# Kernel tuning notes

Hardware: AMD Instinct MI355X
Metric: run time of the kernel (lower is better)

Reference implementation:

```python
import jax, jax.numpy as jnp
import numpy as np

BN_EPS = 1e-5


def setup_inputs() -> dict:
    key = jax.random.key(0)
    ks = jax.random.split(key, 10)
    B, L, V, D = 4096, 200, 100000, 256
    tokens = jax.random.randint(ks[0], (B, L), 0, V, dtype=jnp.int32)
    lengths = jnp.maximum(jax.random.randint(ks[1], (B,), 0, L + 1, dtype=jnp.int32), 1)
    t = (jax.random.uniform(ks[2], (B,)) > 0.5).astype(jnp.float32)
    emb_table = jax.random.normal(ks[3], (V, D), dtype=jnp.float32)
    W1 = jax.random.normal(ks[4], (D, D), dtype=jnp.float32) * (1.0 / np.sqrt(D))
    b1 = jnp.zeros((D,), dtype=jnp.float32)
    gamma = jnp.ones((D,), dtype=jnp.float32)
    beta = jnp.zeros((D,), dtype=jnp.float32)
    w2 = jax.random.normal(ks[5], (D,), dtype=jnp.float32) * (1.0 / np.sqrt(D))
    b2 = jnp.zeros((), dtype=jnp.float32)
    return {"tokens": tokens, "lengths": lengths, "t": t, "emb_table": emb_table,
            "W1": W1, "b1": b1, "gamma": gamma, "beta": beta, "w2": w2, "b2": b2}


def reference(tokens, lengths, t, emb_table, W1, b1, gamma, beta, w2, b2):
    B, L = tokens.shape
    # ragged gather + mean pool (EmbeddingBag-mean equivalent)
    emb = emb_table[tokens]                                   # [B, L, D]
    mask = (jnp.arange(L)[None, :] < lengths[:, None]).astype(emb.dtype)  # [B, L]
    pooled = jnp.einsum('bld,bl->bd', emb, mask) / lengths[:, None].astype(emb.dtype)
    # fc_hidden -> BatchNorm1d (training-mode batch stats) -> ReLU (dropout = eval identity)
    z = pooled @ W1.T + b1                                    # [B, D]
    mu = jnp.mean(z, axis=0)
    var = jnp.var(z, axis=0)
    zn = (z - mu) / jnp.sqrt(var + BN_EPS)
    h = jax.nn.relu(gamma * zn + beta)
    # fc_output -> logits
    logits = h @ w2 + b2                                      # [B]
    # BCEWithLogitsLoss (mean, numerically stable)
    loss = jnp.mean(jnp.maximum(logits, 0.0) - logits * t + jnp.log1p(jnp.exp(-jnp.abs(logits))))
    return (loss, logits)
```

## Files before the change

### kernel.cpp

```cpp
#include <hip/hip_runtime.h>
#include <math.h>

#define L_ 200

__global__ __launch_bounds__(256) void pool_pack_kernel(
    const int* __restrict__ tokens, const int* __restrict__ lengths,
    const float* __restrict__ emb, float* __restrict__ pooled,
    const float* __restrict__ W1, float* __restrict__ W1p) {
  const int tid = threadIdx.x;
  if (blockIdx.x < 64) {
    float4 v = ((const float4*)W1)[tid * 64 + blockIdx.x];
    ((float4*)W1p)[blockIdx.x * 256 + tid] = v;
  }
  const int wv = tid >> 6, lane = tid & 63;
  const int row = blockIdx.x * 2 + (wv >> 1);
  const int half = wv & 1;
  const int len = lengths[row];
  const int* trow = tokens + row * L_;
  const float4* embv = (const float4*)emb;
  float4 a0 = make_float4(0.f, 0.f, 0.f, 0.f);
  float4 a1 = a0, a2 = a0, a3 = a0;
  for (int l0 = half * 64; l0 < len; l0 += 128) {
    int nt = len - l0; nt = nt > 64 ? 64 : nt;
    int tk = (lane < nt) ? trow[l0 + lane] : 0;
    int j = 0;
    for (; j + 4 <= nt; j += 4) {
      int t0 = __shfl(tk, j);
      int t1 = __shfl(tk, j + 1);
      int t2 = __shfl(tk, j + 2);
      int t3 = __shfl(tk, j + 3);
      float4 v0 = embv[(size_t)t0 * 64 + lane];
      float4 v1 = embv[(size_t)t1 * 64 + lane];
      float4 v2 = embv[(size_t)t2 * 64 + lane];
      float4 v3 = embv[(size_t)t3 * 64 + lane];
      a0.x += v0.x; a0.y += v0.y; a0.z += v0.z; a0.w += v0.w;
      a1.x += v1.x; a1.y += v1.y; a1.z += v1.z; a1.w += v1.w;
      a2.x += v2.x; a2.y += v2.y; a2.z += v2.z; a2.w += v2.w;
      a3.x += v3.x; a3.y += v3.y; a3.z += v3.z; a3.w += v3.w;
    }
    for (; j < nt; j++) {
      int t0 = __shfl(tk, j);
      float4 v0 = embv[(size_t)t0 * 64 + lane];
      a0.x += v0.x; a0.y += v0.y; a0.z += v0.z; a0.w += v0.w;
    }
  }
  float4 r;
  r.x = a0.x + a1.x + a2.x + a3.x;
  r.y = a0.y + a1.y + a2.y + a3.y;
  r.z = a0.z + a1.z + a2.z + a3.z;
  r.w = a0.w + a1.w + a2.w + a3.w;
  __shared__ float4 part[2][64];
  if (half) part[wv >> 1][lane] = r;
  __syncthreads();
  if (!half) {
    float4 o = part[wv >> 1][lane];
    const float inv = 1.0f / (float)len;
    r.x = (r.x + o.x) * inv;
    r.y = (r.y + o.y) * inv;
    r.z = (r.z + o.z) * inv;
    r.w = (r.w + o.w) * inv;
    ((float4*)pooled)[(size_t)row * 64 + lane] = r;
  }
}

__global__ __launch_bounds__(256) void gemm_stats_kernel(
    const float* __restrict__ pooled, const float* __restrict__ W1p,
    const float* __restrict__ b1, float* __restrict__ z,
    float* __restrict__ psum, float* __restrict__ psq) {
  __shared__ float4 SH[1024];
  const int tid = threadIdx.x;
  const int b0 = blockIdx.x * 16;
  const float4* pooled4 = (const float4*)pooled;
#pragma unroll
  for (int i = 0; i < 4; i++)
    SH[tid + i * 256] = pooled4[(size_t)b0 * 64 + tid + i * 256];
  __syncthreads();
  const int wv = tid >> 6, lane = tid & 63;
  const int r0 = wv * 4;
  float4 bb = ((const float4*)b1)[lane];
  float acc[4][4];
#pragma unroll
  for (int r = 0; r < 4; r++) {
    acc[r][0] = bb.x; acc[r][1] = bb.y; acc[r][2] = bb.z; acc[r][3] = bb.w;
  }
  const float4* w4 = (const float4*)W1p;
  for (int kb = 0; kb < 64; kb++) {
    float4 wk0 = w4[kb * 256 + lane * 4 + 0];
    float4 wk1 = w4[kb * 256 + lane * 4 + 1];
    float4 wk2 = w4[kb * 256 + lane * 4 + 2];
    float4 wk3 = w4[kb * 256 + lane * 4 + 3];
#pragma unroll
    for (int r = 0; r < 4; r++) {
      float4 p = SH[(r0 + r) * 64 + kb];
      acc[r][0] += p.x * wk0.x + p.y * wk0.y + p.z * wk0.z + p.w * wk0.w;
      acc[r][1] += p.x * wk1.x + p.y * wk1.y + p.z * wk1.z + p.w * wk1.w;
      acc[r][2] += p.x * wk2.x + p.y * wk2.y + p.z * wk2.z + p.w * wk2.w;
      acc[r][3] += p.x * wk3.x + p.y * wk3.y + p.z * wk3.z + p.w * wk3.w;
    }
  }
  float4* z4 = (float4*)z;
  float4 s = make_float4(0.f, 0.f, 0.f, 0.f), q = s;
#pragma unroll
  for (int r = 0; r < 4; r++) {
    float4 o = make_float4(acc[r][0], acc[r][1], acc[r][2], acc[r][3]);
    z4[(size_t)(b0 + r0 + r) * 64 + lane] = o;
    s.x += o.x; s.y += o.y; s.z += o.z; s.w += o.w;
    q.x += o.x * o.x; q.y += o.y * o.y; q.z += o.z * o.z; q.w += o.w * o.w;
  }
  __syncthreads();
  SH[wv * 64 + lane] = s;
  SH[256 + wv * 64 + lane] = q;
  __syncthreads();
  if (tid < 64) {
    float4 S = make_float4(0.f, 0.f, 0.f, 0.f), Q = S;
#pragma unroll
    for (int w = 0; w < 4; w++) {
      float4 a = SH[w * 64 + tid];
      float4 b = SH[256 + w * 64 + tid];
      S.x += a.x; S.y += a.y; S.z += a.z; S.w += a.w;
      Q.x += b.x; Q.y += b.y; Q.z += b.z; Q.w += b.w;
    }
    ((float4*)psum)[blockIdx.x * 64 + tid] = S;
    ((float4*)psq)[blockIdx.x * 64 + tid] = Q;
  }
}

__global__ __launch_bounds__(256) void bn_reduce_kernel(
    const float* __restrict__ psum, const float* __restrict__ psq,
    const float* __restrict__ gamma, const float* __restrict__ beta,
    float* __restrict__ A, float* __restrict__ C) {
  const int t = threadIdx.x;
  const int dd = t & 15, c = t >> 4;
  const int d = blockIdx.x * 16 + dd;
  float s = 0.f, q = 0.f;
#pragma unroll
  for (int i = 0; i < 16; i++) {
    int p = c * 16 + i;
    s += psum[p * 256 + d];
    q += psq[p * 256 + d];
  }
  __shared__ float sl[16][17], ql[16][17];
  sl[c][dd] = s; ql[c][dd] = q;
  __syncthreads();
  if (t < 16) {
    float S = 0.f, Q = 0.f;
#pragma unroll
    for (int c2 = 0; c2 < 16; c2++) { S += sl[c2][t]; Q += ql[c2][t]; }
    int dg = blockIdx.x * 16 + t;
    float m = S * (1.0f / 4096.0f);
    float v = Q * (1.0f / 4096.0f) - m * m;
    float a = gamma[dg] * rsqrtf(v + 1e-5f);
    A[dg] = a;
    C[dg] = beta[dg] - m * a;
  }
}

__global__ __launch_bounds__(256) void head_kernel(
    const float* __restrict__ z, const float* __restrict__ A,
    const float* __restrict__ C, const float* __restrict__ w2,
    const float* __restrict__ b2, const float* __restrict__ t,
    float* __restrict__ out, float* __restrict__ bce) {
  const int tid = threadIdx.x;
  const int wv = tid >> 6, lane = tid & 63;
  const int b = blockIdx.x * 4 + wv;
  float4 A4 = ((const float4*)A)[lane];
  float4 C4 = ((const float4*)C)[lane];
  float4 w24 = ((const float4*)w2)[lane];
  float4 zv = ((const float4*)z)[(size_t)b * 64 + lane];
  float h0 = fmaxf(A4.x * zv.x + C4.x, 0.f);
  float h1 = fmaxf(A4.y * zv.y + C4.y, 0.f);
  float h2 = fmaxf(A4.z * zv.z + C4.z, 0.f);
  float h3 = fmaxf(A4.w * zv.w + C4.w, 0.f);
  float part = h0 * w24.x + h1 * w24.y + h2 * w24.z + h3 * w24.w;
#pragma unroll
  for (int off = 32; off > 0; off >>= 1) part += __shfl_down(part, off);
  if (lane == 0) {
    float logit = part + b2[0];
    out[1 + b] = logit;
    float tb = t[b];
    bce[b] = fmaxf(logit, 0.f) - logit * tb + log1pf(expf(-fabsf(logit)));
  }
}

__global__ __launch_bounds__(256) void loss_kernel(const float* __restrict__ bce,
                                                   float* __restrict__ out) {
  __shared__ float red[4];
  const int tid = threadIdx.x;
  float s = 0.f;
  for (int i = 0; i < 16; i++) s += bce[tid + i * 256];
#pragma unroll
  for (int off = 32; off > 0; off >>= 1) s += __shfl_down(s, off);
  if ((tid & 63) == 0) red[tid >> 6] = s;
  __syncthreads();
  if (tid == 0) out[0] = (red[0] + red[1] + red[2] + red[3]) * (1.0f / 4096.0f);
}

extern "C" void kernel_launch(void* const* d_in, const int* in_sizes, int n_in,
                              void* d_out, int out_size, void* d_ws, size_t ws_size,
                              hipStream_t stream) {
  const int* tokens = (const int*)d_in[0];
  const int* lengths = (const int*)d_in[1];
  const float* t = (const float*)d_in[2];
  const float* emb = (const float*)d_in[3];
  const float* W1 = (const float*)d_in[4];
  const float* b1 = (const float*)d_in[5];
  const float* gamma = (const float*)d_in[6];
  const float* beta = (const float*)d_in[7];
  const float* w2 = (const float*)d_in[8];
  const float* b2 = (const float*)d_in[9];
  float* out = (float*)d_out;

  float* wsf = (float*)d_ws;
  float* pooled = wsf;
  float* z = wsf + 1048576;
  float* W1p = wsf + 2097152;
  float* psum = wsf + 2162688;
  float* psq = wsf + 2228224;
  float* A = wsf + 2293760;
  float* C = wsf + 2294016;
  float* bce = wsf + 2294272;

  pool_pack_kernel<<<2048, 256, 0, stream>>>(tokens, lengths, emb, pooled, W1, W1p);
  gemm_stats_kernel<<<256, 256, 0, stream>>>(pooled, W1p, b1, z, psum, psq);
  bn_reduce_kernel<<<16, 256, 0, stream>>>(psum, psq, gamma, beta, A, C);
  head_kernel<<<1024, 256, 0, stream>>>(z, A, C, w2, b2, t, out, bce);
  loss_kernel<<<1, 256, 0, stream>>>(bce, out);
}
```

Before: 240.8 us.

## Convert embedding table to bf16 each call and fuse BN reduce and loss via atomics

Adds a pass that converts the full fp32 embedding table to bf16 in workspace on every call, then gathers bf16 rows during pooling to halve the gather bytes. The BN statistics reduction and the loss reduction move to atomicAdd, which removes the separate bn_reduce and loss kernels. The conversion reads 102MB and writes 51MB per call, which likely costs more than the roughly 205MB of fp32 gathers it saves. It also lowers embedding precision and makes the float atomic sums order-dependent.

```diff
diff --git a/kernel.cpp b/kernel.cpp
--- a/kernel.cpp
+++ b/kernel.cpp
@@ -3,21 +3,54 @@
 
 #define L_ 200
 
-__global__ __launch_bounds__(256) void pool_pack_kernel(
-    const int* __restrict__ tokens, const int* __restrict__ lengths,
-    const float* __restrict__ emb, float* __restrict__ pooled,
-    const float* __restrict__ W1, float* __restrict__ W1p) {
+__device__ __forceinline__ unsigned f2bf_pair(float a, float b) {
+  union { float f; unsigned u; } ca, cb;
+  ca.f = a; cb.f = b;
+  unsigned ra = (ca.u + 0x7FFFu + ((ca.u >> 16) & 1u)) >> 16;
+  unsigned rb = (cb.u + 0x7FFFu + ((cb.u >> 16) & 1u)) >> 16;
+  return (ra & 0xFFFFu) | ((rb & 0xFFFFu) << 16);
+}
+
+__device__ __forceinline__ float bf_lo(unsigned u) {
+  union { unsigned u; float f; } c; c.u = u << 16; return c.f;
+}
+__device__ __forceinline__ float bf_hi(unsigned u) {
+  union { unsigned u; float f; } c; c.u = u & 0xFFFF0000u; return c.f;
+}
+
+__global__ __launch_bounds__(256) void convert_pack_kernel(
+    const float* __restrict__ emb, uint2* __restrict__ embbf,
+    const float* __restrict__ W1, float* __restrict__ W1p,
+    float* __restrict__ ssum, float* __restrict__ ssq, float* __restrict__ out) {
   const int tid = threadIdx.x;
   if (blockIdx.x < 64) {
     float4 v = ((const float4*)W1)[tid * 64 + blockIdx.x];
     ((float4*)W1p)[blockIdx.x * 256 + tid] = v;
-  }
+  } else if (blockIdx.x == 64) {
+    ssum[tid] = 0.f;
+    ssq[tid] = 0.f;
+    if (tid == 0) out[0] = 0.f;
+  }
+  const float4* e4 = (const float4*)emb;
+  const unsigned N4 = 100000u * 64u;
+  for (unsigned i = blockIdx.x * 256 + tid; i < N4; i += 2048u * 256u) {
+    float4 v = e4[i];
+    uint2 o;
+    o.x = f2bf_pair(v.x, v.y);
+    o.y = f2bf_pair(v.z, v.w);
+    embbf[i] = o;
+  }
+}
+
+__global__ __launch_bounds__(256) void pool_kernel(
+    const int* __restrict__ tokens, const int* __restrict__ lengths,
+    const uint2* __restrict__ embbf, float* __restrict__ pooled) {
+  const int tid = threadIdx.x;
   const int wv = tid >> 6, lane = tid & 63;
   const int row = blockIdx.x * 2 + (wv >> 1);
   const int half = wv & 1;
   const int len = lengths[row];
   const int* trow = tokens + row * L_;
-  const float4* embv = (const float4*)emb;
   float4 a0 = make_float4(0.f, 0.f, 0.f, 0.f);
   float4 a1 = a0, a2 = a0, a3 = a0;
   for (int l0 = half * 64; l0 < len; l0 += 128) {
@@ -29,19 +62,19 @@
       int t1 = __shfl(tk, j + 1);
       int t2 = __shfl(tk, j + 2);
       int t3 = __shfl(tk, j + 3);
-      float4 v0 = embv[(size_t)t0 * 64 + lane];
-      float4 v1 = embv[(size_t)t1 * 64 + lane];
-      float4 v2 = embv[(size_t)t2 * 64 + lane];
-      float4 v3 = embv[(size_t)t3 * 64 + lane];
-      a0.x += v0.x; a0.y += v0.y; a0.z += v0.z; a0.w += v0.w;
-      a1.x += v1.x; a1.y += v1.y; a1.z += v1.z; a1.w += v1.w;
-      a2.x += v2.x; a2.y += v2.y; a2.z += v2.z; a2.w += v2.w;
-      a3.x += v3.x; a3.y += v3.y; a3.z += v3.z; a3.w += v3.w;
+      uint2 v0 = embbf[(size_t)t0 * 64 + lane];
+      uint2 v1 = embbf[(size_t)t1 * 64 + lane];
+      uint2 v2 = embbf[(size_t)t2 * 64 + lane];
+      uint2 v3 = embbf[(size_t)t3 * 64 + lane];
+      a0.x += bf_lo(v0.x); a0.y += bf_hi(v0.x); a0.z += bf_lo(v0.y); a0.w += bf_hi(v0.y);
+      a1.x += bf_lo(v1.x); a1.y += bf_hi(v1.x); a1.z += bf_lo(v1.y); a1.w += bf_hi(v1.y);
+      a2.x += bf_lo(v2.x); a2.y += bf_hi(v2.x); a2.z += bf_lo(v2.y); a2.w += bf_hi(v2.y);
+      a3.x += bf_lo(v3.x); a3.y += bf_hi(v3.x); a3.z += bf_lo(v3.y); a3.w += bf_hi(v3.y);
     }
     for (; j < nt; j++) {
       int t0 = __shfl(tk, j);
-      float4 v0 = embv[(size_t)t0 * 64 + lane];
-      a0.x += v0.x; a0.y += v0.y; a0.z += v0.z; a0.w += v0.w;
+      uint2 v0 = embbf[(size_t)t0 * 64 + lane];
+      a0.x += bf_lo(v0.x); a0.y += bf_hi(v0.x); a0.z += bf_lo(v0.y); a0.w += bf_hi(v0.y);
     }
   }
   float4 r;
@@ -66,7 +99,7 @@
 __global__ __launch_bounds__(256) void gemm_stats_kernel(
     const float* __restrict__ pooled, const float* __restrict__ W1p,
     const float* __restrict__ b1, float* __restrict__ z,
-    float* __restrict__ psum, float* __restrict__ psq) {
+    float* __restrict__ ssum, float* __restrict__ ssq) {
   __shared__ float4 SH[1024];
   const int tid = threadIdx.x;
   const int b0 = blockIdx.x * 16;
@@ -120,52 +153,49 @@
       S.x += a.x; S.y += a.y; S.z += a.z; S.w += a.w;
       Q.x += b.x; Q.y += b.y; Q.z += b.z; Q.w += b.w;
     }
-    ((float4*)psum)[blockIdx.x * 64 + tid] = S;
-    ((float4*)psq)[blockIdx.x * 64 + tid] = Q;
-  }
-}
-
-__global__ __launch_bounds__(256) void bn_reduce_kernel(
-    const float* __restrict__ psum, const float* __restrict__ psq,
-    const float* __restrict__ gamma, const float* __restrict__ beta,
-    float* __restrict__ A, float* __restrict__ C) {
-  const int t = threadIdx.x;
-  const int dd = t & 15, c = t >> 4;
-  const int d = blockIdx.x * 16 + dd;
-  float s = 0.f, q = 0.f;
-#pragma unroll
-  for (int i = 0; i < 16; i++) {
-    int p = c * 16 + i;
-    s += psum[p * 256 + d];
-    q += psq[p * 256 + d];
-  }
-  __shared__ float sl[16][17], ql[16][17];
-  sl[c][dd] = s; ql[c][dd] = q;
-  __syncthreads();
-  if (t < 16) {
-    float S = 0.f, Q = 0.f;
-#pragma unroll
-    for (int c2 = 0; c2 < 16; c2++) { S += sl[c2][t]; Q += ql[c2][t]; }
-    int dg = blockIdx.x * 16 + t;
-    float m = S * (1.0f / 4096.0f);
-    float v = Q * (1.0f / 4096.0f) - m * m;
-    float a = gamma[dg] * rsqrtf(v + 1e-5f);
-    A[dg] = a;
-    C[dg] = beta[dg] - m * a;
-  }
-}
-
-__global__ __launch_bounds__(256) void head_kernel(
-    const float* __restrict__ z, const float* __restrict__ A,
-    const float* __restrict__ C, const float* __restrict__ w2,
+    atomicAdd(&ssum[4 * tid + 0], S.x);
+    atomicAdd(&ssum[4 * tid + 1], S.y);
+    atomicAdd(&ssum[4 * tid + 2], S.z);
+    atomicAdd(&ssum[4 * tid + 3], S.w);
+    atomicAdd(&ssq[4 * tid + 0], Q.x);
+    atomicAdd(&ssq[4 * tid + 1], Q.y);
+    atomicAdd(&ssq[4 * tid + 2], Q.z);
+    atomicAdd(&ssq[4 * tid + 3], Q.w);
+  }
+}
+
+__global__ __launch_bounds__(256) void head_loss_kernel(
+    const float* __restrict__ z, const float* __restrict__ ssum,
+    const float* __restrict__ ssq, const float* __restrict__ gamma,
+    const float* __restrict__ beta, const float* __restrict__ w2,
     const float* __restrict__ b2, const float* __restrict__ t,
-    float* __restrict__ out, float* __restrict__ bce) {
+    float* __restrict__ out) {
   const int tid = threadIdx.x;
   const int wv = tid >> 6, lane = tid & 63;
   const int b = blockIdx.x * 4 + wv;
-  float4 A4 = ((const float4*)A)[lane];
-  float4 C4 = ((const float4*)C)[lane];
+  float4 s4 = ((const float4*)ssum)[lane];
+  float4 q4 = ((const float4*)ssq)[lane];
+  float4 g4 = ((const float4*)gamma)[lane];
+  float4 be4 = ((const float4*)beta)[lane];
   float4 w24 = ((const float4*)w2)[lane];
+  const float invB = 1.0f / 4096.0f;
+  float4 A4, C4;
+  {
+    float m = s4.x * invB, v = q4.x * invB - m * m;
+    float rs = rsqrtf(v + 1e-5f); A4.x = g4.x * rs; C4.x = be4.x - m * A4.x;
+  }
+  {
+    float m = s4.y * invB, v = q4.y * invB - m * m;
+    float rs = rsqrtf(v + 1e-5f); A4.y = g4.y * rs; C4.y = be4.y - m * A4.y;
+  }
+  {
+    float m = s4.z * invB, v = q4.z * invB - m * m;
+    float rs = rsqrtf(v + 1e-5f); A4.z = g4.z * rs; C4.z = be4.z - m * A4.z;
+  }
+  {
+    float m = s4.w * invB, v = q4.w * invB - m * m;
+    float rs = rsqrtf(v + 1e-5f); A4.w = g4.w * rs; C4.w = be4.w - m * A4.w;
+  }
   float4 zv = ((const float4*)z)[(size_t)b * 64 + lane];
   float h0 = fmaxf(A4.x * zv.x + C4.x, 0.f);
   float h1 = fmaxf(A4.y * zv.y + C4.y, 0.f);
@@ -174,25 +204,16 @@
   float part = h0 * w24.x + h1 * w24.y + h2 * w24.z + h3 * w24.w;
 #pragma unroll
   for (int off = 32; off > 0; off >>= 1) part += __shfl_down(part, off);
+  __shared__ float red[4];
   if (lane == 0) {
     float logit = part + b2[0];
     out[1 + b] = logit;
     float tb = t[b];
-    bce[b] = fmaxf(logit, 0.f) - logit * tb + log1pf(expf(-fabsf(logit)));
-  }
-}
-
-__global__ __launch_bounds__(256) void loss_kernel(const float* __restrict__ bce,
-                                                   float* __restrict__ out) {
-  __shared__ float red[4];
-  const int tid = threadIdx.x;
-  float s = 0.f;
-  for (int i = 0; i < 16; i++) s += bce[tid + i * 256];
-#pragma unroll
-  for (int off = 32; off > 0; off >>= 1) s += __shfl_down(s, off);
-  if ((tid & 63) == 0) red[tid >> 6] = s;
-  __syncthreads();
-  if (tid == 0) out[0] = (red[0] + red[1] + red[2] + red[3]) * (1.0f / 4096.0f);
+    red[wv] = fmaxf(logit, 0.f) - logit * tb + log1pf(expf(-fabsf(logit)));
+  }
+  __syncthreads();
+  if (tid == 0)
+    atomicAdd(out, (red[0] + red[1] + red[2] + red[3]) * (1.0f / 4096.0f));
 }
 
 extern "C" void kernel_launch(void* const* d_in, const int* in_sizes, int n_in,
@@ -211,18 +232,15 @@
   float* out = (float*)d_out;
 
   float* wsf = (float*)d_ws;
-  float* pooled = wsf;
-  float* z = wsf + 1048576;
-  float* W1p = wsf + 2097152;
-  float* psum = wsf + 2162688;
-  float* psq = wsf + 2228224;
-  float* A = wsf + 2293760;
-  float* C = wsf + 2294016;
-  float* bce = wsf + 2294272;
-
-  pool_pack_kernel<<<2048, 256, 0, stream>>>(tokens, lengths, emb, pooled, W1, W1p);
-  gemm_stats_kernel<<<256, 256, 0, stream>>>(pooled, W1p, b1, z, psum, psq);
-  bn_reduce_kernel<<<16, 256, 0, stream>>>(psum, psq, gamma, beta, A, C);
-  head_kernel<<<1024, 256, 0, stream>>>(z, A, C, w2, b2, t, out, bce);
-  loss_kernel<<<1, 256, 0, stream>>>(bce, out);
-}
+  uint2* embbf = (uint2*)d_ws;
+  float* pooled = wsf + 12800000;
+  float* z = wsf + 13848576;
+  float* W1p = wsf + 14897152;
+  float* ssum = wsf + 14962688;
+  float* ssq = wsf + 14962944;
+
+  convert_pack_kernel<<<2048, 256, 0, stream>>>(emb, embbf, W1, W1p, ssum, ssq, out);
+  pool_kernel<<<2048, 256, 0, stream>>>(tokens, lengths, embbf, pooled);
+  gemm_stats_kernel<<<256, 256, 0, stream>>>(pooled, W1p, b1, z, ssum, ssq);
+  head_loss_kernel<<<1024, 256, 0, stream>>>(z, ssum, ssq, gamma, beta, w2, b2, t, out);
+}
```

New measurement: 280.7 us. +16.5%, slower.
